# Kernel optimization log

Hardware: AMD Instinct MI355X
Metric: run time of the kernel (lower is better)

Reference implementation:

```python
import jax, jax.numpy as jnp
import numpy as np

EPS = 1e-5
COMMIT_W = 2.0
LATENT = 64


def _conv1d(x, w, b, stride, padding):
    # x: [B,C,T], w: [O,I,K] (torch Conv1d layout)
    y = jax.lax.conv_general_dilated(x, w, (stride,), [(padding, padding)],
                                     dimension_numbers=('NCH', 'OIH', 'NCH'))
    return y + b[None, :, None]


def _bn(x, g, b):
    # training-mode BatchNorm1d: batch statistics over (B, T) per channel
    mu = x.mean(axis=(0, 2), keepdims=True)
    var = x.var(axis=(0, 2), keepdims=True)
    return (x - mu) * jax.lax.rsqrt(var + EPS) * g[None, :, None] + b[None, :, None]


def setup_inputs():
    key = jax.random.key(0)
    ks = jax.random.split(key, 10)
    B, T, D, K = 8, 10240, LATENT, 8192
    f32 = jnp.float32
    def n(k, shape, scale):
        return jax.random.normal(k, shape, dtype=f32) * scale
    return {
        'x': jax.random.normal(ks[0], (B, 1, T), dtype=f32),
        'enc_w1': n(ks[1], (16, 1, 5), 0.3), 'enc_b1': jnp.zeros((16,), f32),
        'bn1_g': jnp.ones((16,), f32), 'bn1_b': jnp.zeros((16,), f32),
        'enc_w2': n(ks[2], (32, 16, 5), 0.1), 'enc_b2': jnp.zeros((32,), f32),
        'bn2_g': jnp.ones((32,), f32), 'bn2_b': jnp.zeros((32,), f32),
        'enc_w3': n(ks[3], (64, 32, 25), 0.05), 'enc_b3': jnp.zeros((64,), f32),
        'bn3_g': jnp.ones((64,), f32), 'bn3_b': jnp.zeros((64,), f32),
        'codebook': jax.random.normal(ks[4], (K, D), dtype=f32),
        'dec_wt': n(ks[5], (64, 64, 25), 0.05),  # torch ConvTranspose1d [in,out,k]
        'dbn1_g': jnp.ones((64,), f32), 'dbn1_b': jnp.zeros((64,), f32),
        'dec_w2': n(ks[6], (64, 64, 5), 0.08), 'dec_b2': jnp.zeros((64,), f32),
        'dbn2_g': jnp.ones((64,), f32), 'dbn2_b': jnp.zeros((64,), f32),
        'dec_w3': n(ks[7], (1, 64, 1), 0.1), 'dec_b3': jnp.zeros((1,), f32),
    }


def reference(x, enc_w1, enc_b1, bn1_g, bn1_b, enc_w2, enc_b2, bn2_g, bn2_b,
              enc_w3, enc_b3, bn3_g, bn3_b, codebook, dec_wt, dbn1_g, dbn1_b,
              dec_w2, dec_b2, dbn2_g, dbn2_b, dec_w3, dec_b3):
    # ---- encoder ----
    h = jax.nn.silu(_conv1d(x, enc_w1, enc_b1, 1, 2))
    h = _bn(h, bn1_g, bn1_b)
    h = jax.nn.silu(_conv1d(h, enc_w2, enc_b2, 1, 2))
    h = _bn(h, bn2_g, bn2_b)
    h = jnp.tanh(_conv1d(h, enc_w3, enc_b3, 5, 12))
    z = _bn(h, bn3_g, bn3_b)                       # [B, 64, L]
    B, _, L = z.shape
    # ---- VQ: euclidean nearest-neighbor against codebook ----
    zf = z.transpose(0, 2, 1).reshape(-1, LATENT)  # [N, D]
    d = ((zf * zf).sum(-1, keepdims=True)
         - 2.0 * zf @ codebook.T
         + (codebook * codebook).sum(-1)[None, :])  # [N, K]
    idx = jnp.argmin(d, axis=-1)                   # [N]
    q = codebook[idx]                              # [N, D]
    commit_loss = COMMIT_W * jnp.mean((jax.lax.stop_gradient(q) - zf) ** 2)
    q_st = zf + jax.lax.stop_gradient(q - zf)      # straight-through
    zq = q_st.reshape(B, L, LATENT).transpose(0, 2, 1)  # [B, 64, L]
    # ---- decoder ----
    # ConvTranspose1d(k=25, s=5, p=12) == dilated conv with flipped kernel
    wconv = jnp.flip(dec_wt, -1).transpose(1, 0, 2)     # [out, in, k]
    h = jax.lax.conv_general_dilated(zq, wconv, (1,), [(12, 12)], lhs_dilation=(5,),
                                     dimension_numbers=('NCH', 'OIH', 'NCH'))
    h = jax.nn.silu(h)
    h = _bn(h, dbn1_g, dbn1_b)
    h = jax.nn.silu(_conv1d(h, dec_w2, dec_b2, 1, 2))
    h = _bn(h, dbn2_g, dbn2_b)
    recon = _conv1d(h, dec_w3, dec_b3, 1, 0)       # [B, 1, ~T]
    T = x.shape[2]
    cur = recon.shape[2]
    if cur > T:
        recon = recon[:, :, :T]
    elif cur < T:
        recon = jnp.pad(recon, ((0, 0), (0, 0), (0, T - cur)))
    return recon, idx.reshape(B, L), commit_loss
```

## Files before the change

kernel.cpp:

```cpp
#include <hip/hip_runtime.h>
#include <hip/hip_bf16.h>

#define DEV __device__ __forceinline__

typedef __attribute__((ext_vector_type(8))) short s8v;
typedef __attribute__((ext_vector_type(16))) float f32x16;
typedef __attribute__((address_space(1))) const unsigned int u32g;
typedef __attribute__((address_space(3))) unsigned int u32l;

DEV void gl_lds(const void* g, void* l){
  __builtin_amdgcn_global_load_lds((u32g*)g, (u32l*)l, 16, 0, 0);
}

DEV float siluf(float x){ return x / (1.f + expf(-x)); }

DEV float wredsum(float v){
  #pragma unroll
  for(int m = 32; m; m >>= 1) v += __shfl_xor(v, m);
  return v;
}

DEV unsigned short bf16rne(float f){
  unsigned int u = __float_as_uint(f);
  u += 0x7FFFu + ((u >> 16) & 1u);
  return (unsigned short)(u >> 16);
}
DEV float bf16tof(unsigned short h){ return __uint_as_float(((unsigned int)h) << 16); }

DEV unsigned umed3(unsigned a, unsigned b, unsigned c){
  unsigned d;
  asm("v_med3_u32 %0, %1, %2, %3" : "=v"(d) : "v"(a), "v"(b), "v"(c));
  return d;
}

#define S1 0
#define Q1 16
#define S2 32
#define Q2 64
#define S3 96
#define Q3 160
#define S4 224
#define Q4 288
#define S5 352
#define Q5 416
#define SLOSS 480
#define NSTATF 512

#define EPSQ 6u
#define NCHUNK 8

__global__ void k_prep(const float* ew3, const float* dwt, float* w3t8,
                       unsigned short* wb7){
  const int n1 = 64*32*25, n2 = 64*64*25;
  for(int i = blockIdx.x*blockDim.x + threadIdx.x; i < n1+n2; i += gridDim.x*blockDim.x){
    if(i < n1){
      int c = i/(32*25), r = i - c*(32*25), ii = r/25, k = r - ii*25;
      int kk = k % 5, kap = k / 5;
      w3t8[(((size_t)(ii*5 + kk))*64 + c)*8 + kap] = ew3[i];
    } else {
      int j = i - n1;
      int ii = j/(64*25), r = j - ii*(64*25), o = r/25, k = r - o*25;
      wb7[((size_t)(k*64 + o))*64 + ii] = bf16rne(dwt[j]);
    }
  }
}

__global__ void k_prep2(const float* __restrict__ cb, unsigned short* __restrict__ cbsw,
                        float* __restrict__ cnw, float* __restrict__ cnw2,
                        unsigned short* __restrict__ cbb, int* cnt){
  if(blockIdx.x == 0 && threadIdx.x == 0) *cnt = 0;
  int j = blockIdx.x*256 + threadIdx.x;
  if(j < 8192){
    float nrm = 0.f;
    unsigned swz = (j & 15) << 4;
    char* rowp = (char*)cbsw + (size_t)j*256;
    #pragma unroll
    for(int k = 0; k < 64; k++){
      float x = cb[(size_t)j*64 + k];
      unsigned short hi = bf16rne(x);
      float lo = x - bf16tof(hi);
      *(unsigned short*)(rowp + (((unsigned)(2*k)) ^ swz)) = hi;
      *(unsigned short*)(rowp + (((unsigned)(128 + 2*k)) ^ swz)) = bf16rne(lo);
      cbb[(size_t)j*64 + k] = hi;
      nrm = fmaf(x, x, nrm);
    }
    cnw[j] = nrm;
    cnw2[j] = (nrm + 1024.f) * 256.f;
  }
}

__global__ void k1(const float* __restrict__ x, const float* __restrict__ w1,
                   const float* __restrict__ b1, float* __restrict__ h1, float* stats){
  __shared__ float xs[136];
  __shared__ float ssum[16], ssq[16];
  int tid = threadIdx.x, b = blockIdx.y, t0 = blockIdx.x*128;
  if(tid < 16){ ssum[tid] = 0.f; ssq[tid] = 0.f; }
  for(int i = tid; i < 132; i += 256){
    int t = t0 + i - 2;
    xs[i] = (t >= 0 && t < 10240) ? x[b*10240 + t] : 0.f;
  }
  __syncthreads();
  int c = tid & 15, sgrp = tid >> 4;
  float w[5];
  #pragma unroll
  for(int k = 0; k < 5; k++) w[k] = w1[c*5 + k];
  float bias = b1[c];
  float outv[8];
  float ps = 0.f, pq = 0.f;
  #pragma unroll
  for(int s = 0; s < 8; s++){
    float a = bias;
    #pragma unroll
    for(int k = 0; k < 5; k++) a = fmaf(w[k], xs[sgrp*8 + s + k], a);
    a = siluf(a);
    outv[s] = a;
    ps += a; pq += a*a;
  }
  float* op = h1 + ((size_t)(b*16 + c))*10240 + t0 + sgrp*8;
  #pragma unroll
  for(int q = 0; q < 2; q++)
    *(float4*)(op + q*4) = make_float4(outv[q*4], outv[q*4+1], outv[q*4+2], outv[q*4+3]);
  ps += __shfl_xor(ps, 16); pq += __shfl_xor(pq, 16);
  ps += __shfl_xor(ps, 32); pq += __shfl_xor(pq, 32);
  if((tid & 48) == 0){ atomicAdd(&ssum[c], ps); atomicAdd(&ssq[c], pq); }
  __syncthreads();
  if(tid < 16){ atomicAdd(stats+S1+tid, ssum[tid]); atomicAdd(stats+Q1+tid, ssq[tid]); }
}

__global__ __launch_bounds__(256) void k2(const float* __restrict__ h1,
                   const float* __restrict__ w2, const float* __restrict__ b2,
                   const float* __restrict__ g1, const float* __restrict__ bb1,
                   float* __restrict__ h2out, float* stats){
  __shared__ float hs[16][136];
  __shared__ float A1s[16], B1s[16];
  __shared__ float ssum[32], ssq[32];
  int tid = threadIdx.x, b = blockIdx.y, t0 = blockIdx.x*128;
  if(tid < 16){
    float mu = stats[S1+tid]/81920.f;
    float var = stats[Q1+tid]/81920.f - mu*mu;
    float rs = rsqrtf(var + 1e-5f);
    A1s[tid] = rs*g1[tid];
    B1s[tid] = bb1[tid] - mu*rs*g1[tid];
  }
  if(tid < 32){ ssum[tid] = 0.f; ssq[tid] = 0.f; }
  __syncthreads();
  {
    int ch = tid >> 4, j0 = tid & 15;
    float A = A1s[ch], B = B1s[ch];
    const float* hp = h1 + ((size_t)(b*16 + ch))*10240;
    for(int j = j0; j < 132; j += 16){
      int t = t0 + j - 2;
      hs[ch][j] = (t >= 0 && t < 10240) ? hp[t]*A + B : 0.f;
    }
  }
  __syncthreads();
  int c = tid & 31, tgrp = tid >> 5;
  int tb = tgrp*16;
  float acc[16];
  float bias = b2[c];
  #pragma unroll
  for(int s = 0; s < 16; s++) acc[s] = bias;
  for(int ic = 0; ic < 4; ic++){
    float wf[20];
    const float* wp = w2 + c*80 + ic*20;
    #pragma unroll
    for(int q = 0; q < 5; q++) *(float4*)(wf + q*4) = *(const float4*)(wp + q*4);
    #pragma unroll
    for(int di = 0; di < 4; di++){
      int i = ic*4 + di;
      float z[20];
      #pragma unroll
      for(int q = 0; q < 5; q++) *(float4*)(z + q*4) = *(const float4*)(&hs[i][tb] + q*4);
      float w0 = wf[di*5], w1 = wf[di*5+1], w2v = wf[di*5+2], w3 = wf[di*5+3], w4 = wf[di*5+4];
      #pragma unroll
      for(int s = 0; s < 16; s++)
        acc[s] = fmaf(w0, z[s], fmaf(w1, z[s+1], fmaf(w2v, z[s+2],
                 fmaf(w3, z[s+3], fmaf(w4, z[s+4], acc[s])))));
    }
  }
  float ps = 0.f, pq = 0.f;
  #pragma unroll
  for(int s = 0; s < 16; s++){
    float a = siluf(acc[s]);
    acc[s] = a;
    ps += a; pq += a*a;
  }
  float* op = h2out + ((size_t)(b*32 + c))*10240 + t0 + tb;
  #pragma unroll
  for(int q = 0; q < 4; q++)
    *(float4*)(op + q*4) = make_float4(acc[q*4], acc[q*4+1], acc[q*4+2], acc[q*4+3]);
  ps += __shfl_xor(ps, 32); pq += __shfl_xor(pq, 32);
  if((tid & 32) == 0){ atomicAdd(&ssum[c], ps); atomicAdd(&ssq[c], pq); }
  __syncthreads();
  if(tid < 32){ atomicAdd(stats+S2+tid, ssum[tid]); atomicAdd(stats+Q2+tid, ssq[tid]); }
}

__global__ void k3(const float* __restrict__ h2, const float* __restrict__ w3t8,
                   const float* __restrict__ eb3, const float* __restrict__ g2,
                   const float* __restrict__ bb2, float* __restrict__ zn, float* stats){
  __shared__ __align__(16) float X[5*32*40];
  __shared__ float A2[32], B2[32];
  __shared__ float ssum[64], ssq[64];
  int tid = threadIdx.x, b = blockIdx.y, l0 = blockIdx.x*32;
  if(tid < 32){
    float mu = stats[S2+tid]/81920.f;
    float var = stats[Q2+tid]/81920.f - mu*mu;
    float rs = rsqrtf(var + 1e-5f);
    A2[tid] = rs*g2[tid];
    B2[tid] = bb2[tid] - mu*rs*g2[tid];
  }
  if(tid < 64){ ssum[tid] = 0.f; ssq[tid] = 0.f; }
  __syncthreads();
  for(int i2 = tid; i2 < 5*32*36; i2 += 256){
    int kk = i2/1152;
    int r  = i2 - kk*1152;
    int ch = r/36, m = r - ch*36;
    int t = 5*(l0 + m) + kk - 12;
    float v = 0.f;
    if(t >= 0 && t < 10240) v = h2[((b*32+ch)*10240)+t]*A2[ch] + B2[ch];
    X[(kk*32+ch)*40 + m] = v;
  }
  __syncthreads();
  int c = tid & 63, lslot = tid >> 6;
  float acc[8];
  float bias = eb3[c];
  #pragma unroll
  for(int s = 0; s < 8; s++) acc[s] = bias;
  for(int i = 0; i < 32; i++){
    #pragma unroll
    for(int kk = 0; kk < 5; kk++){
      const float* xp = &X[(kk*32+i)*40 + lslot*8];
      float z[12];
      #pragma unroll
      for(int q = 0; q < 3; q++) *(float4*)(z + q*4) = *(const float4*)(xp + q*4);
      const float* wp = w3t8 + (((size_t)(i*5 + kk))*64 + c)*8;
      float wv[5];
      *(float4*)wv = *(const float4*)wp;
      wv[4] = wp[4];
      #pragma unroll
      for(int kap = 0; kap < 5; kap++){
        float w = wv[kap];
        #pragma unroll
        for(int s = 0; s < 8; s++) acc[s] = fmaf(w, z[s+kap], acc[s]);
      }
    }
  }
  float ls = 0.f, lq = 0.f;
  #pragma unroll
  for(int s = 0; s < 8; s++){
    int l = l0 + lslot*8 + s;
    float a = tanhf(acc[s]);
    zn[((b*2048 + l)*64) + c] = a;
    ls += a; lq += a*a;
  }
  atomicAdd(&ssum[c], ls); atomicAdd(&ssq[c], lq);
  __syncthreads();
  if(tid < 64){ atomicAdd(stats+S3+tid, ssum[tid]); atomicAdd(stats+Q3+tid, ssq[tid]); }
}

__global__ __launch_bounds__(256, 4) void k5m(const float* __restrict__ zn,
    const unsigned short* __restrict__ cbsw, const float* __restrict__ cnw2,
    const float* __restrict__ g3, const float* __restrict__ b3,
    const float* __restrict__ stats,
    unsigned int* __restrict__ pbk, unsigned int* __restrict__ psk){
  __shared__ __align__(16) unsigned char cbuf[2][16384];
  __shared__ float A3s[64], B3s[64];
  int tid = threadIdx.x;
  int chunk = blockIdx.x;
  int m0 = blockIdx.y * 128;
  int lane = tid & 63, wr = tid >> 6;
  int h = lane >> 5, cll = lane & 31;
  int row = m0 + wr*32 + cll;

  if(tid < 64){
    float mu = stats[S3+tid]/16384.f;
    float var = stats[Q3+tid]/16384.f - mu*mu;
    float rs = rsqrtf(var + 1e-5f);
    A3s[tid] = rs*g3[tid];
    B3s[tid] = b3[tid] - mu*rs*g3[tid];
  }

  int c0 = chunk * 1024;
  const char* csrc = (const char*)cbsw + (size_t)c0*256;
  #pragma unroll
  for(int c2 = 0; c2 < 4; c2++)
    gl_lds(csrc + c2*4096 + tid*16, &cbuf[0][0] + c2*4096 + tid*16);
  __syncthreads();

  s8v ah[4], al[4];
  const float* zp = zn + (size_t)row*64;
  #pragma unroll
  for(int s = 0; s < 4; s++){
    int koff = s*16 + h*8;
    float4 v0 = *(const float4*)(zp + koff);
    float4 v1 = *(const float4*)(zp + koff + 4);
    float vv[8] = {v0.x,v0.y,v0.z,v0.w,v1.x,v1.y,v1.z,v1.w};
    #pragma unroll
    for(int i = 0; i < 8; i++){
      float v = fmaf(vv[i], A3s[koff + i], B3s[koff + i]);
      unsigned short hi = bf16rne(v);
      ah[s][i] = (short)hi;
      al[s][i] = (short)bf16rne(v - bf16tof(hi));
    }
  }

  unsigned int bk[16], sk[16];
  #pragma unroll
  for(int r = 0; r < 16; r++){ bk[r] = 0xFFFFFFFFu; sk[r] = 0xFFFFFFFFu; }
  f32x16 zv;
  #pragma unroll
  for(int i = 0; i < 16; i++) zv[i] = 0.f;

  unsigned swz = (unsigned)(cll & 15) << 4;
  for(int tile = 0; tile < 16; ++tile){
    int bsel = tile & 1;
    if(tile < 15){
      const char* ns = csrc + (size_t)(tile+1)*16384;
      #pragma unroll
      for(int c2 = 0; c2 < 4; c2++)
        gl_lds(ns + c2*4096 + tid*16, &cbuf[bsel^1][0] + c2*4096 + tid*16);
    }
    #pragma unroll
    for(int half = 0; half < 2; half++){
      const unsigned char* bp = &cbuf[bsel][0] + (half*32 + cll)*256;
      s8v bh[4], bl[4];
      #pragma unroll
      for(int s = 0; s < 4; s++){
        bh[s] = *(const s8v*)(bp + (((unsigned)(s*32 + h*16)) ^ swz));
        bl[s] = *(const s8v*)(bp + (((unsigned)(128 + s*32 + h*16)) ^ swz));
      }
      unsigned col = (unsigned)(c0 + tile*64 + half*32 + cll);
      float cnv2 = cnw2[col];
      f32x16 a = __builtin_amdgcn_mfma_f32_32x32x16_bf16(ah[0], bl[0], zv, 0, 0, 0);
      a = __builtin_amdgcn_mfma_f32_32x32x16_bf16(al[0], bh[0], a, 0, 0, 0);
      a = __builtin_amdgcn_mfma_f32_32x32x16_bf16(ah[0], bh[0], a, 0, 0, 0);
      #pragma unroll
      for(int s = 1; s < 4; s++){
        a = __builtin_amdgcn_mfma_f32_32x32x16_bf16(ah[s], bl[s], a, 0, 0, 0);
        a = __builtin_amdgcn_mfma_f32_32x32x16_bf16(al[s], bh[s], a, 0, 0, 0);
        a = __builtin_amdgcn_mfma_f32_32x32x16_bf16(ah[s], bh[s], a, 0, 0, 0);
      }
      #pragma unroll
      for(int r = 0; r < 16; r++){
        float q = fmaf(-512.f, a[r], cnv2);
        q = fminf(q, 524287.f);
        unsigned k = (((unsigned)q) << 13) | col;
        unsigned nb = bk[r] < k ? bk[r] : k;
        sk[r] = umed3(sk[r], bk[r], k);
        bk[r] = nb;
      }
    }
    __syncthreads();
  }

  #pragma unroll
  for(int m = 1; m <= 16; m <<= 1){
    #pragma unroll
    for(int r = 0; r < 16; r++){
      unsigned int ob = (unsigned int)__shfl_xor((int)bk[r], m);
      unsigned int os = (unsigned int)__shfl_xor((int)sk[r], m);
      unsigned int s2 = sk[r] < os ? sk[r] : os;
      sk[r] = umed3(s2, bk[r], ob);
      bk[r] = bk[r] < ob ? bk[r] : ob;
    }
  }
  if(cll == 0){
    size_t base = (size_t)chunk*16384 + m0 + wr*32 + 4*h;
    #pragma unroll
    for(int r = 0; r < 16; r++){
      int lr = (r&3) + 8*(r>>2);
      pbk[base + lr] = bk[r];
      psk[base + lr] = sk[r];
    }
  }
}

__global__ void k5r(const unsigned int* __restrict__ pbk,
                    const unsigned int* __restrict__ psk, int* __restrict__ idxw,
                    float* __restrict__ out_idx, int* __restrict__ list, int* cnt){
  int row = blockIdx.x*256 + threadIdx.x;
  unsigned int bk = pbk[row], sk = psk[row];
  #pragma unroll
  for(int c = 1; c < NCHUNK; c++){
    unsigned int ob = pbk[(size_t)c*16384 + row];
    unsigned int os = psk[(size_t)c*16384 + row];
    unsigned int s2 = sk < os ? sk : os;
    sk = umed3(s2, bk, ob);
    bk = bk < ob ? bk : ob;
  }
  int idx = (int)(bk & 0x1FFFu);
  idxw[row] = idx;
  out_idx[row] = (float)idx;
  if((sk >> 13) - (bk >> 13) <= EPSQ){
    int p = atomicAdd(cnt, 1);
    list[p] = row;
  }
}

__global__ __launch_bounds__(256) void k5x(const float* __restrict__ zn,
    const float* __restrict__ cb, const float* __restrict__ cnw,
    const float* __restrict__ g3, const float* __restrict__ b3,
    const float* __restrict__ stats,
    const int* __restrict__ list, const int* cnt,
    float* __restrict__ pxd, int* __restrict__ pxi){
  __shared__ float A3s[64], B3s[64];
  int tid = threadIdx.x;
  if(tid < 64){
    float mu = stats[S3+tid]/16384.f;
    float var = stats[Q3+tid]/16384.f - mu*mu;
    float rs = rsqrtf(var + 1e-5f);
    A3s[tid] = rs*g3[tid];
    B3s[tid] = b3[tid] - mu*rs*g3[tid];
  }
  __syncthreads();
  int chunk = blockIdx.x;
  int n = *cnt;
  int rgrp = tid >> 6, cs = tid & 63;
  int c0 = chunk * 1024;
  for(int bat = blockIdx.y; bat*4 < n; bat += 256){
    int e = bat*4 + rgrp;
    int ec = e < n ? e : n-1;
    int row = list[ec];
    float4 zr[16];
    const float4* zp = (const float4*)(zn + (size_t)row*64);
    #pragma unroll
    for(int q = 0; q < 16; q++){
      float4 v = zp[q];
      v.x = fmaf(v.x, A3s[q*4+0], B3s[q*4+0]);
      v.y = fmaf(v.y, A3s[q*4+1], B3s[q*4+1]);
      v.z = fmaf(v.z, A3s[q*4+2], B3s[q*4+2]);
      v.w = fmaf(v.w, A3s[q*4+3], B3s[q*4+3]);
      zr[q] = v;
    }
    float bd = 3.4e38f; int bi = 0;
    for(int step = 0; step < 16; step++){
      int j = c0 + step*64 + cs;
      const float4* cp = (const float4*)(cb + (size_t)j*64);
      float cnv = cnw[j];
      float da = 0.f, db = 0.f;
      #pragma unroll
      for(int q = 0; q < 16; q += 2){
        float4 ca = cp[q], cb4 = cp[q+1];
        da = fmaf(ca.x, zr[q].x, da);  da = fmaf(ca.y, zr[q].y, da);
        da = fmaf(ca.z, zr[q].z, da);  da = fmaf(ca.w, zr[q].w, da);
        db = fmaf(cb4.x, zr[q+1].x, db); db = fmaf(cb4.y, zr[q+1].y, db);
        db = fmaf(cb4.z, zr[q+1].z, db); db = fmaf(cb4.w, zr[q+1].w, db);
      }
      float d = fmaf(-2.f, da + db, cnv);
      if(d < bd){ bd = d; bi = j; }
    }
    #pragma unroll
    for(int m = 1; m <= 32; m <<= 1){
      float od = __shfl_xor(bd, m);
      int   oi = __shfl_xor(bi, m);
      if(od < bd || (od == bd && oi < bi)){ bd = od; bi = oi; }
    }
    if(cs == 0 && e < n){
      pxd[(size_t)chunk*16384 + e] = bd;
      pxi[(size_t)chunk*16384 + e] = bi;
    }
  }
}

__global__ void k5x2(const float* __restrict__ pxd, const int* __restrict__ pxi,
                     const int* __restrict__ list, const int* cnt,
                     int* __restrict__ idxw, float* __restrict__ out_idx){
  int e = blockIdx.x*256 + threadIdx.x;
  int n = *cnt;
  if(e >= n) return;
  float bd = pxd[e]; int bi = pxi[e];
  #pragma unroll
  for(int c = 1; c < NCHUNK; c++){
    float od = pxd[(size_t)c*16384 + e];
    int   oi = pxi[(size_t)c*16384 + e];
    if(od < bd || (od == bd && oi < bi)){ bd = od; bi = oi; }
  }
  int row = list[e];
  idxw[row] = bi;
  out_idx[row] = (float)bi;
}

__global__ void k_loss(const float* __restrict__ zn, const float* __restrict__ cb,
                       const float* __restrict__ g3, const float* __restrict__ b3,
                       const int* __restrict__ idxw, float* stats){
  __shared__ float A3s[64], B3s[64];
  int tid = threadIdx.x;
  if(tid < 64){
    float mu = stats[S3+tid]/16384.f;
    float var = stats[Q3+tid]/16384.f - mu*mu;
    float rs = rsqrtf(var + 1e-5f);
    A3s[tid] = rs*g3[tid];
    B3s[tid] = b3[tid] - mu*rs*g3[tid];
  }
  __syncthreads();
  int row = blockIdx.x*256 + tid;
  int code = idxw[row];
  const float* cp = cb + (size_t)code*64;
  const float* zp = zn + (size_t)row*64;
  float s = 0.f;
  #pragma unroll
  for(int k = 0; k < 64; k++){
    float v = fmaf(zp[k], A3s[k], B3s[k]);
    float dd = cp[k] - v;
    s = fmaf(dd, dd, s);
  }
  float tot = wredsum(s);
  if((tid & 63) == 0) atomicAdd(stats + SLOSS, tot);
}

__global__ __launch_bounds__(320) void k7m(const int* __restrict__ idxp,
    const unsigned short* __restrict__ cbb, const unsigned short* __restrict__ wb7,
    unsigned short* __restrict__ h4t, float* stats){
  __shared__ __align__(16) unsigned char lA[37*128];
  __shared__ float tb[5*64*33];
  __shared__ float ssum[64], ssq[64];
  int tid = threadIdx.x, b = blockIdx.y, u0 = blockIdx.x*32;
  if(tid < 64){ ssum[tid] = 0.f; ssq[tid] = 0.f; }
  {
    int m = tid >> 3, part = tid & 7;
    if(m < 37){
      int u = u0 - 2 + m;
      uint4 val = make_uint4(0,0,0,0);
      if(u >= 0 && u < 2048){
        int code = idxp[b*2048 + u];
        val = *(const uint4*)((const char*)cbb + (size_t)code*128 + part*16);
      }
      *(uint4*)(lA + m*128 + (((unsigned)(part*16)) ^ (((unsigned)m & 7) << 4))) = val;
    }
  }
  __syncthreads();
  int lane = tid & 63, h = lane >> 5, cl = lane & 31;
  int v = tid >> 6;
  const int km[5]  = {2,3,4,0,1};
  const int ovv[5] = {2,2,2,3,3};
  f32x16 acc0, acc1;
  #pragma unroll
  for(int i = 0; i < 16; i++){ acc0[i] = 0.f; acc1[i] = 0.f; }
  #pragma unroll
  for(int r = 0; r < 5; r++){
    int off = ovv[v] - r + 2;
    int m = cl + off;
    unsigned aswz = ((unsigned)m & 7) << 4;
    int k = km[v] + 5*r;
    const char* b0p = (const char*)wb7 + (size_t)(k*64 + cl)*128;
    const char* b1p = b0p + 32*128;
    #pragma unroll
    for(int s = 0; s < 4; s++){
      unsigned o = (unsigned)(s*32 + h*16);
      s8v a  = *(const s8v*)(lA + m*128 + (o ^ aswz));
      s8v b0 = *(const s8v*)(b0p + o);
      s8v b1 = *(const s8v*)(b1p + o);
      acc0 = __builtin_amdgcn_mfma_f32_32x32x16_bf16(a, b0, acc0, 0, 0, 0);
      acc1 = __builtin_amdgcn_mfma_f32_32x32x16_bf16(a, b1, acc1, 0, 0, 0);
    }
  }
  float ps0 = 0.f, pq0 = 0.f, ps1 = 0.f, pq1 = 0.f;
  #pragma unroll
  for(int r = 0; r < 16; r++){
    int ul = (r&3) + 8*(r>>2) + 4*h;
    int u = u0 + ul;
    float v0 = siluf(acc0[r]), v1 = siluf(acc1[r]);
    tb[(v*64 + cl)*33 + ul]      = v0;
    tb[(v*64 + 32 + cl)*33 + ul] = v1;
    if(v == 0 || u < 2047){ ps0 += v0; pq0 += v0*v0; ps1 += v1; pq1 += v1*v1; }
  }
  atomicAdd(&ssum[cl], ps0);      atomicAdd(&ssq[cl], pq0);
  atomicAdd(&ssum[32 + cl], ps1); atomicAdd(&ssq[32 + cl], pq1);
  __syncthreads();
  if(tid < 64){ atomicAdd(stats+S4+tid, ssum[tid]); atomicAdd(stats+Q4+tid, ssq[tid]); }
  #pragma unroll
  for(int j = 0; j < 16; j++){
    int flat = j*320 + tid;
    int tl = flat >> 5;
    int chp = flat & 31;
    int t = u0*5 + tl;
    if(t < 10236){
      int vv = tl % 5, ul = tl / 5;
      float f0 = tb[(vv*64 + 2*chp)*33 + ul];
      float f1 = tb[(vv*64 + 2*chp + 1)*33 + ul];
      unsigned int pk = (unsigned int)bf16rne(f0) | ((unsigned int)bf16rne(f1) << 16);
      size_t rowb = ((size_t)b*10248 + 2 + t)*128;
      *(unsigned int*)((char*)h4t + rowb + (((unsigned)(4*chp)) ^ (((unsigned)t & 7) << 4))) = pk;
    }
  }
}

__global__ void k8w(const float* __restrict__ w2d, const float* __restrict__ b2d,
                    const float* __restrict__ g4, const float* __restrict__ bb4,
                    const float* __restrict__ stats, unsigned short* __restrict__ wbt,
                    float* __restrict__ beta, unsigned int* __restrict__ h4tz){
  __shared__ float A4[64], B4[64];
  int tid = threadIdx.x;
  for(int i = tid; i < 3072; i += 256){
    int b = i / 384, r = i - b*384;
    int row12 = r >> 5, word = r & 31;
    int row = row12 < 2 ? row12 : 10236 + row12;
    h4tz[((size_t)b*10248 + row)*32 + word] = 0u;
  }
  if(tid < 64){
    float mu = stats[S4+tid]/81888.f;
    float var = stats[Q4+tid]/81888.f - mu*mu;
    float rs = rsqrtf(var + 1e-5f);
    A4[tid] = rs*g4[tid];
    B4[tid] = bb4[tid] - mu*rs*g4[tid];
  }
  __syncthreads();
  for(int e = tid; e < 64*64*5; e += 256){
    int c = e/320, r = e - c*320, i = r/5, k = r - i*5;
    unsigned short hw = bf16rne(w2d[e] * A4[i]);
    int row = k*64 + c;
    *(unsigned short*)((char*)wbt + (size_t)row*128 + (((unsigned)(2*i)) ^ (((unsigned)c & 7) << 4))) = hw;
  }
  if(tid < 64){
    float s = b2d[tid];
    for(int i = 0; i < 64; i++){
      float wsum = 0.f;
      #pragma unroll
      for(int k = 0; k < 5; k++) wsum += w2d[(tid*64 + i)*5 + k];
      s += wsum * B4[i];
    }
    beta[tid] = s;
  }
}

__global__ __launch_bounds__(256) void k8(const unsigned short* __restrict__ h4t,
    const unsigned short* __restrict__ wbt, const float* __restrict__ beta,
    unsigned short* __restrict__ h5b, float* stats){
  __shared__ __align__(16) unsigned char lA[68*128];
  __shared__ float ssum[64], ssq[64];
  int tid = threadIdx.x, b = blockIdx.y, t0 = blockIdx.x*64;
  if(tid < 64){ ssum[tid] = 0.f; ssq[tid] = 0.f; }
  const char* srcA = (const char*)h4t + ((size_t)b*10248 + t0)*128;
  #pragma unroll
  for(int c2 = 0; c2 < 2; c2++)
    gl_lds(srcA + c2*4096 + tid*16, lA + c2*4096 + tid*16);
  if(tid < 32) gl_lds(srcA + 8192 + tid*16, lA + 8192 + tid*16);
  __syncthreads();

  int lane = tid & 63, h = lane >> 5, cl = lane & 31;
  int widx = tid >> 6;
  int wt0 = (widx >> 1) * 32;
  int wch = (widx & 1) * 32;
  f32x16 acc;
  #pragma unroll
  for(int i = 0; i < 16; i++) acc[i] = 0.f;
  unsigned bswz = (unsigned)(cl & 7) << 4;
  #pragma unroll
  for(int k = 0; k < 5; k++){
    int l = wt0 + cl + k;
    unsigned aswz = (unsigned)((l + 6) & 7) << 4;
    const char* bp = (const char*)wbt + (size_t)(k*64 + wch + cl)*128;
    #pragma unroll
    for(int s = 0; s < 4; s++){
      unsigned o = (unsigned)(s*32 + h*16);
      s8v a  = *(const s8v*)(lA + l*128 + (o ^ aswz));
      s8v bb = *(const s8v*)(bp + (o ^ bswz));
      acc = __builtin_amdgcn_mfma_f32_32x32x16_bf16(a, bb, acc, 0, 0, 0);
    }
  }
  float bet = beta[wch + cl];
  float ps = 0.f, pq = 0.f;
  #pragma unroll
  for(int r = 0; r < 16; r++){
    int t = t0 + wt0 + (r&3) + 8*(r>>2) + 4*h;
    float v0 = siluf(acc[r] + bet);
    if(t < 10236){
      h5b[((size_t)b*10240 + t)*64 + wch + cl] = bf16rne(v0);
      ps += v0; pq += v0*v0;
    }
  }
  atomicAdd(&ssum[wch + cl], ps); atomicAdd(&ssq[wch + cl], pq);
  __syncthreads();
  if(tid < 64){ atomicAdd(stats+S5+tid, ssum[tid]); atomicAdd(stats+Q5+tid, ssq[tid]); }
}

__global__ void k9(const unsigned short* __restrict__ h5b, const float* __restrict__ w3,
                   const float* __restrict__ b3, const float* __restrict__ g5,
                   const float* __restrict__ bb5, const float* stats,
                   float* __restrict__ out){
  __shared__ float WA[64], WB[64];
  int tid = threadIdx.x;
  if(blockIdx.x == 0 && blockIdx.y == 0 && tid == 0)
    out[98304] = 2.f * stats[SLOSS] / 1048576.f;
  if(tid < 64){
    float mu = stats[S5+tid]/81888.f;
    float var = stats[Q5+tid]/81888.f - mu*mu;
    float rs = rsqrtf(var + 1e-5f);
    float A = rs*g5[tid], B = bb5[tid] - mu*rs*g5[tid];
    float w = w3[tid];
    WA[tid] = w*A; WB[tid] = w*B;
  }
  __syncthreads();
  int b = blockIdx.y;
  int t = blockIdx.x*256 + tid;
  float acc = b3[0];
  if(t < 10236){
    const unsigned short* hp = h5b + ((size_t)b*10240 + t)*64;
    #pragma unroll
    for(int q = 0; q < 8; q++){
      uint4 u = *(const uint4*)(hp + q*8);
      unsigned int ua[4] = {u.x, u.y, u.z, u.w};
      #pragma unroll
      for(int w = 0; w < 4; w++){
        int c = q*8 + w*2;
        acc += WA[c]*bf16tof((unsigned short)(ua[w] & 0xFFFFu)) + WB[c];
        acc += WA[c+1]*bf16tof((unsigned short)(ua[w] >> 16)) + WB[c+1];
      }
    }
  } else acc = 0.f;
  out[b*10240 + t] = acc;
}

extern "C" void kernel_launch(void* const* d_in, const int* in_sizes, int n_in,
                              void* d_out, int out_size, void* d_ws, size_t ws_size,
                              hipStream_t stream){
  const float* x   = (const float*)d_in[0];
  const float* ew1 = (const float*)d_in[1];
  const float* eb1 = (const float*)d_in[2];
  const float* g1  = (const float*)d_in[3];
  const float* bb1 = (const float*)d_in[4];
  const float* ew2 = (const float*)d_in[5];
  const float* eb2 = (const float*)d_in[6];
  const float* g2  = (const float*)d_in[7];
  const float* bb2 = (const float*)d_in[8];
  const float* ew3 = (const float*)d_in[9];
  const float* eb3 = (const float*)d_in[10];
  const float* g3  = (const float*)d_in[11];
  const float* bb3 = (const float*)d_in[12];
  const float* cb  = (const float*)d_in[13];
  const float* dwt = (const float*)d_in[14];
  const float* g4  = (const float*)d_in[15];
  const float* bb4 = (const float*)d_in[16];
  const float* w2d = (const float*)d_in[17];
  const float* b2d = (const float*)d_in[18];
  const float* g5  = (const float*)d_in[19];
  const float* bb5 = (const float*)d_in[20];
  const float* w3d = (const float*)d_in[21];
  const float* b3d = (const float*)d_in[22];

  char* ws = (char*)d_ws;
  float* h1   = (float*)(ws + 0);
  unsigned short* cbsw = (unsigned short*)(ws + 0);
  float* cnw  = (float*)(ws + 2097152);
  float* cnw2 = (float*)(ws + 2129920);
  float* h2   = (float*)(ws + 5242880);
  float* zn   = (float*)(ws + 15728640);
  unsigned short* h4t = (unsigned short*)(ws + 0);
  unsigned short* h5b = (unsigned short*)(ws + 20971520);
  int*   list = (int*)  (ws + 20971520);
  int*   cnt  = (int*)  (ws + 21037056);
  unsigned int* pbk = (unsigned int*)(ws + 21037312);
  unsigned int* psk = (unsigned int*)(ws + 21561600);
  float* pxd  = (float*)(ws + 22085888);
  int*   pxi  = (int*)  (ws + 22610176);
  unsigned short* wbt = (unsigned short*)(ws + 31457280);
  float* beta = (float*)(ws + 31498240);
  unsigned short* wb7 = (unsigned short*)(ws + 32000000);
  unsigned short* cbb = (unsigned short*)(ws + 32300032);
  float* w3t8 = (float*)(ws + 41934848);
  int*   idxw = (int*)  (ws + 42549248);
  float* stats= (float*)(ws + 42614784);
  if(ws_size < 42616832) return;

  float* out = (float*)d_out;

  hipMemsetAsync(stats, 0, NSTATF*4, stream);
  k_prep<<<600, 256, 0, stream>>>(ew3, dwt, w3t8, wb7);
  k1<<<dim3(80,8), 256, 0, stream>>>(x, ew1, eb1, h1, stats);
  k2<<<dim3(80,8), 256, 0, stream>>>(h1, ew2, eb2, g1, bb1, h2, stats);
  k_prep2<<<32, 256, 0, stream>>>(cb, cbsw, cnw, cnw2, cbb, cnt);
  k3<<<dim3(64,8), 256, 0, stream>>>(h2, w3t8, eb3, g2, bb2, zn, stats);
  k5m<<<dim3(NCHUNK,128), 256, 0, stream>>>(zn, cbsw, cnw2, g3, bb3, stats, pbk, psk);
  k5r<<<64, 256, 0, stream>>>(pbk, psk, idxw, out + 81920, list, cnt);
  k5x<<<dim3(NCHUNK,256), 256, 0, stream>>>(zn, cb, cnw, g3, bb3, stats, list, cnt, pxd, pxi);
  k5x2<<<64, 256, 0, stream>>>(pxd, pxi, list, cnt, idxw, out + 81920);
  k_loss<<<64, 256, 0, stream>>>(zn, cb, g3, bb3, idxw, stats);
  k7m<<<dim3(64,8), 320, 0, stream>>>(idxw, cbb, wb7, h4t, stats);
  k8w<<<1, 256, 0, stream>>>(w2d, b2d, g4, bb4, stats, wbt, beta, (unsigned int*)h4t);
  k8<<<dim3(160,8), 256, 0, stream>>>(h4t, wbt, beta, h5b, stats);
  k9<<<dim3(40,8), 256, 0, stream>>>(h5b, w3d, b3d, g5, bb5, stats, out);
}
```

Measured before the change: 337.4 us.

## Fold BN2 affine into conv3 weights and bias, read h2 directly

Adds a k3w kernel that scales the conv3 weights by the BN2 scale and folds the BN2 shift into a per-channel bias. Zero padding is emulated by a per-channel pad value (-B/A), so that after folding it still acts as a zero input. k3 no longer stages a normalized tile in LDS: each thread loads 60 contiguous h2 samples per input channel straight from global memory into registers. This removes the LDS staging, its sync and the per-element normalization, but adds a small extra launch, more register pressure from z[60], and redundant global reads across threads that depend on cache. The pad trick is only valid when the BN scale is nonzero.

```diff
diff --git a/kernel.cpp b/kernel.cpp
--- a/kernel.cpp
+++ b/kernel.cpp
@@ -49,19 +49,11 @@
 #define EPSQ 6u
 #define NCHUNK 8
 
-__global__ void k_prep(const float* ew3, const float* dwt, float* w3t8,
-                       unsigned short* wb7){
-  const int n1 = 64*32*25, n2 = 64*64*25;
-  for(int i = blockIdx.x*blockDim.x + threadIdx.x; i < n1+n2; i += gridDim.x*blockDim.x){
-    if(i < n1){
-      int c = i/(32*25), r = i - c*(32*25), ii = r/25, k = r - ii*25;
-      int kk = k % 5, kap = k / 5;
-      w3t8[(((size_t)(ii*5 + kk))*64 + c)*8 + kap] = ew3[i];
-    } else {
-      int j = i - n1;
-      int ii = j/(64*25), r = j - ii*(64*25), o = r/25, k = r - o*25;
-      wb7[((size_t)(k*64 + o))*64 + ii] = bf16rne(dwt[j]);
-    }
+__global__ void k_prep(const float* dwt, unsigned short* wb7){
+  const int n2 = 64*64*25;
+  for(int j = blockIdx.x*blockDim.x + threadIdx.x; j < n2; j += gridDim.x*blockDim.x){
+    int ii = j/(64*25), r = j - ii*(64*25), o = r/25, k = r - o*25;
+    wb7[((size_t)(k*64 + o))*64 + ii] = bf16rne(dwt[j]);
   }
 }
 
@@ -195,13 +187,13 @@
   if(tid < 32){ atomicAdd(stats+S2+tid, ssum[tid]); atomicAdd(stats+Q2+tid, ssq[tid]); }
 }
 
-__global__ void k3(const float* __restrict__ h2, const float* __restrict__ w3t8,
-                   const float* __restrict__ eb3, const float* __restrict__ g2,
-                   const float* __restrict__ bb2, float* __restrict__ zn, float* stats){
-  __shared__ __align__(16) float X[5*32*40];
+__global__ void k3w(const float* __restrict__ ew3, const float* __restrict__ eb3,
+                    const float* __restrict__ g2, const float* __restrict__ bb2,
+                    const float* __restrict__ stats, float* __restrict__ w3f8,
+                    float* __restrict__ cbias, float* __restrict__ zpad){
   __shared__ float A2[32], B2[32];
-  __shared__ float ssum[64], ssq[64];
-  int tid = threadIdx.x, b = blockIdx.y, l0 = blockIdx.x*32;
+  __shared__ float red[256];
+  int tid = threadIdx.x;
   if(tid < 32){
     float mu = stats[S2+tid]/81920.f;
     float var = stats[Q2+tid]/81920.f - mu*mu;
@@ -209,39 +201,74 @@
     A2[tid] = rs*g2[tid];
     B2[tid] = bb2[tid] - mu*rs*g2[tid];
   }
+  __syncthreads();
+  if(blockIdx.x < 200){
+    int e = blockIdx.x*256 + tid;
+    int kap = e % 5; int r = e / 5;
+    int c = r & 63; r >>= 6;
+    int kk = r % 5; int i = r / 5;
+    float w = ew3[c*800 + i*25 + kap*5 + kk];
+    w3f8[(((size_t)(i*5 + kk))*64 + c)*8 + kap] = w * A2[i];
+  } else {
+    if(tid < 32){
+      float a = A2[tid];
+      zpad[tid] = (fabsf(a) > 1e-30f) ? (-B2[tid] / a) : 0.f;
+    }
+    int c = tid & 63, ig = tid >> 6;
+    float s = 0.f;
+    for(int i = ig*8; i < ig*8 + 8; i++){
+      float wsum = 0.f;
+      #pragma unroll
+      for(int k = 0; k < 25; k++) wsum += ew3[c*800 + i*25 + k];
+      s += wsum * B2[i];
+    }
+    red[tid] = s;
+    __syncthreads();
+    if(tid < 64) cbias[tid] = eb3[tid] + red[tid] + red[tid+64] + red[tid+128] + red[tid+192];
+  }
+}
+
+__global__ __launch_bounds__(256) void k3(const float* __restrict__ h2,
+                   const float* __restrict__ w3f8, const float* __restrict__ cbias,
+                   const float* __restrict__ zpad,
+                   float* __restrict__ zn, float* stats){
+  __shared__ float ssum[64], ssq[64];
+  int tid = threadIdx.x, b = blockIdx.y, l0 = blockIdx.x*32;
   if(tid < 64){ ssum[tid] = 0.f; ssq[tid] = 0.f; }
   __syncthreads();
-  for(int i2 = tid; i2 < 5*32*36; i2 += 256){
-    int kk = i2/1152;
-    int r  = i2 - kk*1152;
-    int ch = r/36, m = r - ch*36;
-    int t = 5*(l0 + m) + kk - 12;
-    float v = 0.f;
-    if(t >= 0 && t < 10240) v = h2[((b*32+ch)*10240)+t]*A2[ch] + B2[ch];
-    X[(kk*32+ch)*40 + m] = v;
-  }
-  __syncthreads();
   int c = tid & 63, lslot = tid >> 6;
+  int tbase = 5*(l0 + lslot*8) - 12;
+  bool edge = (blockIdx.x == 0) || (blockIdx.x == 63);
   float acc[8];
-  float bias = eb3[c];
-  #pragma unroll
-  for(int s = 0; s < 8; s++) acc[s] = bias;
+  float cb0 = cbias[c];
+  #pragma unroll
+  for(int s = 0; s < 8; s++) acc[s] = cb0;
   for(int i = 0; i < 32; i++){
+    const float* hp = h2 + ((size_t)(b*32 + i))*10240;
+    float z[60];
+    if(edge){
+      float zp_i = zpad[i];
+      #pragma unroll
+      for(int e = 0; e < 60; e++){
+        int t = tbase + e;
+        z[e] = (t >= 0 && t < 10240) ? hp[t] : zp_i;
+      }
+    } else {
+      #pragma unroll
+      for(int q = 0; q < 15; q++)
+        *(float4*)(z + q*4) = *(const float4*)(hp + tbase + q*4);
+    }
     #pragma unroll
     for(int kk = 0; kk < 5; kk++){
-      const float* xp = &X[(kk*32+i)*40 + lslot*8];
-      float z[12];
-      #pragma unroll
-      for(int q = 0; q < 3; q++) *(float4*)(z + q*4) = *(const float4*)(xp + q*4);
-      const float* wp = w3t8 + (((size_t)(i*5 + kk))*64 + c)*8;
-      float wv[5];
-      *(float4*)wv = *(const float4*)wp;
-      wv[4] = wp[4];
+      const float* wp = w3f8 + (((size_t)(i*5 + kk))*64 + c)*8;
+      float w[5];
+      *(float4*)w = *(const float4*)wp;
+      w[4] = wp[4];
       #pragma unroll
       for(int kap = 0; kap < 5; kap++){
-        float w = wv[kap];
         #pragma unroll
-        for(int s = 0; s < 8; s++) acc[s] = fmaf(w, z[s+kap], acc[s]);
+        for(int s = 0; s < 8; s++)
+          acc[s] = fmaf(w[kap], z[5*(s+kap) + kk], acc[s]);
       }
     }
   }
@@ -757,7 +784,9 @@
   float* beta = (float*)(ws + 31498240);
   unsigned short* wb7 = (unsigned short*)(ws + 32000000);
   unsigned short* cbb = (unsigned short*)(ws + 32300032);
-  float* w3t8 = (float*)(ws + 41934848);
+  float* w3f8 = (float*)(ws + 33400000);
+  float* cbias= (float*)(ws + 42139648);
+  float* zpad = (float*)(ws + 42139904);
   int*   idxw = (int*)  (ws + 42549248);
   float* stats= (float*)(ws + 42614784);
   if(ws_size < 42616832) return;
@@ -765,11 +794,12 @@
   float* out = (float*)d_out;
 
   hipMemsetAsync(stats, 0, NSTATF*4, stream);
-  k_prep<<<600, 256, 0, stream>>>(ew3, dwt, w3t8, wb7);
+  k_prep<<<400, 256, 0, stream>>>(dwt, wb7);
   k1<<<dim3(80,8), 256, 0, stream>>>(x, ew1, eb1, h1, stats);
   k2<<<dim3(80,8), 256, 0, stream>>>(h1, ew2, eb2, g1, bb1, h2, stats);
   k_prep2<<<32, 256, 0, stream>>>(cb, cbsw, cnw, cnw2, cbb, cnt);
-  k3<<<dim3(64,8), 256, 0, stream>>>(h2, w3t8, eb3, g2, bb2, zn, stats);
+  k3w<<<201, 256, 0, stream>>>(ew3, eb3, g2, bb2, stats, w3f8, cbias, zpad);
+  k3<<<dim3(64,8), 256, 0, stream>>>(h2, w3f8, cbias, zpad, zn, stats);
   k5m<<<dim3(NCHUNK,128), 256, 0, stream>>>(zn, cbsw, cnw2, g3, bb3, stats, pbk, psk);
   k5r<<<64, 256, 0, stream>>>(pbk, psk, idxw, out + 81920, list, cnt);
   k5x<<<dim3(NCHUNK,256), 256, 0, stream>>>(zn, cb, cnw, g3, bb3, stats, list, cnt, pxd, pxi);
```

New measurement: 383.7 us. 1.14x slower.
